# Kernel optimization log

Measured on AMD Instinct MI355X. Metric: run time of the kernel, lower is better.

The kernel has to match this reference:

```python
import jax, jax.numpy as jnp
import numpy as np

B, L, E, H, DV, V = 256, 512, 200, 256, 30000, 50000
NEG_INF = -jnp.inf

def setup_inputs() -> dict:
    key = jax.random.key(0)
    ks = jax.random.split(key, 16)
    s = 0.05
    f = jnp.float32
    return {
        "input_id": jax.random.randint(ks[0], (B, 1), 0, V),
        "input_emb": jax.random.normal(ks[1], (B, 1, E), f),
        "encoder_outputs": jax.random.normal(ks[2], (B, L, H), f),
        "encoder_input_ids": jax.random.randint(ks[3], (B, L), 0, V),
        "hidden": jax.random.normal(ks[4], (B, 1, H), f),
        "attention": jax.random.normal(ks[5], (B, 1, H), f),
        # GRU (PyTorch layout): W_ih (3H, 2H+E), W_hh (3H, H), gate order r,z,n
        "W_ih": jax.random.normal(ks[6], (3 * H, 2 * H + E), f) * s,
        "W_hh": jax.random.normal(ks[7], (3 * H, H), f) * s,
        "b_ih": jnp.zeros((3 * H,), f),
        "b_hh": jnp.zeros((3 * H,), f),
        "W_attn": jax.random.normal(ks[8], (H, H), f) * s,
        "b_attn": jnp.zeros((H,), f),
        "W_comb": jax.random.normal(ks[9], (H, 2 * H), f) * s,
        "b_comb": jnp.zeros((H,), f),
        "W_gen": jax.random.normal(ks[10], (DV, H), f) * s,
        "b_gen": jnp.zeros((DV,), f),
        "W_copy": jax.random.normal(ks[11], (H, H), f) * s,
        "b_copy": jnp.zeros((H,), f),
    }


def reference(input_id, input_emb, encoder_outputs, encoder_input_ids, hidden,
              attention, W_ih, W_hh, b_ih, b_hh, W_attn, b_attn, W_comb,
              b_comb, W_gen, b_gen, W_copy, b_copy):
    b, l = encoder_input_ids.shape
    # selective read: rou = normalized match mask (NaN guard -> 0)
    mask = (input_id == encoder_input_ids).astype(encoder_outputs.dtype)  # (b,l)
    msum = jnp.sum(mask, axis=1, keepdims=True)
    rou = jnp.where(msum > 0, mask / jnp.where(msum > 0, msum, 1.0), 0.0)
    selective_read = jnp.einsum('bl,blh->bh', rou, encoder_outputs)  # (b,h)

    # GRU single step (dropout is identity at inference)
    x = jnp.concatenate([input_emb[:, 0], attention[:, 0], selective_read], axis=-1)
    h_prev = hidden[:, 0]  # (b,h)
    gx = x @ W_ih.T + b_ih          # (b,3h)
    gh = h_prev @ W_hh.T + b_hh     # (b,3h)
    xr, xz, xn = jnp.split(gx, 3, axis=-1)
    hr, hz, hn = jnp.split(gh, 3, axis=-1)
    r = jax.nn.sigmoid(xr + hr)
    z = jax.nn.sigmoid(xz + hz)
    n = jnp.tanh(xn + r * hn)
    h = (1.0 - z) * n + z * h_prev  # (b,h) cur_hidden

    # attention
    q = h @ W_attn.T + b_attn
    attn_w = jax.nn.softmax(jnp.einsum('bh,blh->bl', q, encoder_outputs), axis=-1)
    attn_applied = jnp.einsum('bl,blh->bh', attn_w, encoder_outputs)
    cur_attention = jnp.tanh(
        jnp.concatenate([attn_applied, h], axis=-1) @ W_comb.T + b_comb)  # (b,h)

    # generate + copy scores, joint softmax
    generate_score = cur_attention @ W_gen.T + b_gen                     # (b,DV)
    copy_weights = jax.nn.sigmoid(encoder_outputs @ W_copy.T + b_copy)   # (b,l,h)
    copy_score = jnp.einsum('blh,bh->bl', copy_weights, cur_attention)   # (b,l)
    score = jax.nn.softmax(jnp.concatenate([generate_score, copy_score], axis=1), axis=1)
    gen_s, copy_s = score[:, :DV], score[:, DV:]

    # fused equivalent of the one-hot scatter/mix: direct scatter-add into vocab
    output = jnp.zeros((b, V), score.dtype)
    output = output.at[:, :DV].add(gen_s)
    output = output.at[jnp.arange(b)[:, None], encoder_input_ids].add(copy_s)

    pos = output > 0
    out = jnp.where(pos, jnp.log(jnp.where(pos, output, 1.0)), NEG_INF)
    return out, h[:, None, :], cur_attention[:, None, :]
```

## Files before the change

kernel.cpp:

```cpp
#include <hip/hip_runtime.h>
#include <cmath>

#define B_  256
#define L_  512
#define E_  200
#define H_  256
#define DV_ 30000
#define V_  50000
#define X_  712
#define G3_ 768
#define NT_ 235

#define NEG_BIG -1.0e30f

typedef __attribute__((ext_vector_type(8))) _Float16 half8;
typedef __attribute__((ext_vector_type(4))) float   floatx4;

#define GLOAD16(gptr, lptr)                                                            \
    __builtin_amdgcn_global_load_lds(                                                  \
        (const __attribute__((address_space(1))) unsigned int*)(gptr),                 \
        (__attribute__((address_space(3))) unsigned int*)(lptr), 16, 0, 0)

__global__ void k_selread(const int* __restrict__ input_id, const float* __restrict__ emb,
                          const float* __restrict__ attention, const float* __restrict__ hidden,
                          const float* __restrict__ enc, const int* __restrict__ enc_ids,
                          const float* __restrict__ Wc, _Float16* __restrict__ wcb,
                          float* __restrict__ xT) {
    int b = blockIdx.x, t = threadIdx.x;
    __shared__ int cnt;
    __shared__ int list[L_];
    if (t == 0) cnt = 0;
    __syncthreads();
    wcb[b * H_ + t] = (_Float16)Wc[b * H_ + t];
    int id = input_id[b];
    for (int l = t; l < L_; l += 256) {
        if (enc_ids[b * L_ + l] == id) { int p = atomicAdd(&cnt, 1); list[p] = l; }
    }
    __syncthreads();
    int n = cnt;
    float s = 0.f;
    for (int i = 0; i < n; i++) s += enc[(b * L_ + list[i]) * H_ + t];
    float sel = (n > 0) ? s / (float)n : 0.f;
    for (int k = t; k < E_; k += 256) xT[k * B_ + b] = emb[b * E_ + k];
    xT[(E_ + t) * B_ + b]       = attention[b * H_ + t];
    xT[(E_ + H_ + t) * B_ + b]  = sel;
    xT[(X_ + t) * B_ + b]       = hidden[b * H_ + t];
}

template<int K, int OS>
__global__ void __launch_bounds__(256) k_gru_one(const float* __restrict__ xTp, const float* __restrict__ W,
                                                 const float* __restrict__ bias, float* __restrict__ g) {
    __shared__ __align__(16) float Ws[8 * K];
    int t  = threadIdx.x;
    int j0 = blockIdx.x * 8;
    int bq = t & 63;
    int jh = t >> 6;
#pragma unroll
    for (int jj = 0; jj < 8; jj++) {
        const float4* src = (const float4*)(W + (size_t)(j0 + jj) * K);
        float4* dst = (float4*)(Ws + jj * K);
        for (int i = t; i < K / 4; i += 256) dst[i] = src[i];
    }
    __syncthreads();
    float acc0[4] = {0.f, 0.f, 0.f, 0.f};
    float acc1[4] = {0.f, 0.f, 0.f, 0.f};
    const float* w0 = Ws + (jh * 2 + 0) * K;
    const float* w1 = Ws + (jh * 2 + 1) * K;
#pragma unroll 2
    for (int k4 = 0; k4 < K / 4; k4++) {
        float4 wa = *(const float4*)(w0 + k4 * 4);
        float4 wb = *(const float4*)(w1 + k4 * 4);
        float wav[4] = {wa.x, wa.y, wa.z, wa.w};
        float wbv[4] = {wb.x, wb.y, wb.z, wb.w};
#pragma unroll
        for (int u = 0; u < 4; u++) {
            float4 xv = *(const float4*)(xTp + (size_t)(k4 * 4 + u) * B_ + bq * 4);
            acc0[0] += wav[u] * xv.x; acc0[1] += wav[u] * xv.y;
            acc0[2] += wav[u] * xv.z; acc0[3] += wav[u] * xv.w;
            acc1[0] += wbv[u] * xv.x; acc1[1] += wbv[u] * xv.y;
            acc1[2] += wbv[u] * xv.z; acc1[3] += wbv[u] * xv.w;
        }
    }
    int ja = j0 + jh * 2, jb = ja + 1;
    float ba = bias[ja], bb = bias[jb];
#pragma unroll
    for (int i = 0; i < 4; i++) {
        g[(size_t)(bq * 4 + i) * OS + ja] = acc0[i] + ba;
        g[(size_t)(bq * 4 + i) * OS + jb] = acc1[i] + bb;
    }
}

__global__ void k_gru_gates(const float* __restrict__ gx, const float* __restrict__ gh,
                            const float* __restrict__ hidden, float* __restrict__ hws,
                            float* __restrict__ hT, float* __restrict__ hout) {
    int b = blockIdx.x, j = threadIdx.x;
    float xr = gx[b * G3_ + j], xz = gx[b * G3_ + 256 + j], xn = gx[b * G3_ + 512 + j];
    float hr = gh[b * G3_ + j], hz = gh[b * G3_ + 256 + j], hn = gh[b * G3_ + 512 + j];
    float r = 1.f / (1.f + expf(-(xr + hr)));
    float z = 1.f / (1.f + expf(-(xz + hz)));
    float n = tanhf(xn + r * hn);
    float hp = hidden[b * H_ + j];
    float h = (1.f - z) * n + z * hp;
    hws[b * H_ + j] = h;
    hT[j * B_ + b]  = h;
    hout[b * H_ + j] = h;
}

#define NC_ 4
#define CR_ 128
__global__ void __launch_bounds__(256) k_attn_a(const float* __restrict__ qws, const float* __restrict__ enc,
                         float* __restrict__ avp, float* __restrict__ mdp) {
    int blk = blockIdx.x;
    int b = blk >> 2, c = blk & 3;
    int t = threadIdx.x, lane = t & 63, w = t >> 6;
    __shared__ float ps[CR_];
    __shared__ float red[8];
    const float* encc = enc + ((size_t)b * L_ + c * CR_) * H_;
    float4 q4 = *(const float4*)&qws[b * H_ + lane * 4];
    for (int i = 0; i < 32; i += 8) {
        float s[8];
#pragma unroll
        for (int u = 0; u < 8; u++) {
            float4 e = *(const float4*)(encc + (size_t)(w * 32 + i + u) * H_ + lane * 4);
            s[u] = q4.x * e.x + q4.y * e.y + q4.z * e.z + q4.w * e.w;
        }
#pragma unroll
        for (int u = 0; u < 8; u++) {
#pragma unroll
            for (int o = 1; o < 64; o <<= 1) s[u] += __shfl_xor(s[u], o);
            if (lane == 0) ps[w * 32 + i + u] = s[u];
        }
    }
    __syncthreads();
    {
        float v = ps[w * 32 + (lane & 31)];
#pragma unroll
        for (int o = 1; o < 64; o <<= 1) v = fmaxf(v, __shfl_xor(v, o));
        if (lane == 0) red[w] = v;
    }
    __syncthreads();
    float M = fmaxf(fmaxf(red[0], red[1]), fmaxf(red[2], red[3]));
    float e = (t < CR_) ? __expf(ps[t] - M) : 0.f;
    {
        float ssum = e;
#pragma unroll
        for (int o = 1; o < 64; o <<= 1) ssum += __shfl_xor(ssum, o);
        if (lane == 0) red[4 + w] = ssum;
    }
    __syncthreads();
    if (t < CR_) ps[t] = e;
    if (t == 0) {
        mdp[blk * 2]     = M;
        mdp[blk * 2 + 1] = red[4] + red[5] + red[6] + red[7];
    }
    __syncthreads();
    float a0 = 0.f, a1 = 0.f, a2 = 0.f, a3 = 0.f;
#pragma unroll 4
    for (int r = 0; r < CR_; r += 4) {
        a0 += ps[r + 0] * encc[(size_t)(r + 0) * H_ + t];
        a1 += ps[r + 1] * encc[(size_t)(r + 1) * H_ + t];
        a2 += ps[r + 2] * encc[(size_t)(r + 2) * H_ + t];
        a3 += ps[r + 3] * encc[(size_t)(r + 3) * H_ + t];
    }
    avp[(size_t)blk * H_ + t] = (a0 + a1) + (a2 + a3);
}

__global__ void __launch_bounds__(256) k_attn_b(const float* __restrict__ avp, const float* __restrict__ mdp,
                         const float* __restrict__ hws, const float* __restrict__ W_comb,
                         const float* __restrict__ b_comb,
                         float* __restrict__ caws, _Float16* __restrict__ cab,
                         float* __restrict__ caout) {
    int b = blockIdx.x, t = threadIdx.x;
    __shared__ __align__(16) float xs[2 * H_];
    float m0 = mdp[(b * 4 + 0) * 2], d0 = mdp[(b * 4 + 0) * 2 + 1];
    float m1 = mdp[(b * 4 + 1) * 2], d1 = mdp[(b * 4 + 1) * 2 + 1];
    float m2 = mdp[(b * 4 + 2) * 2], d2 = mdp[(b * 4 + 2) * 2 + 1];
    float m3 = mdp[(b * 4 + 3) * 2], d3 = mdp[(b * 4 + 3) * 2 + 1];
    float M = fmaxf(fmaxf(m0, m1), fmaxf(m2, m3));
    float f0 = __expf(m0 - M), f1 = __expf(m1 - M), f2 = __expf(m2 - M), f3 = __expf(m3 - M);
    float den = f0 * d0 + f1 * d1 + f2 * d2 + f3 * d3;
    float num = f0 * avp[((size_t)b * 4 + 0) * H_ + t] + f1 * avp[((size_t)b * 4 + 1) * H_ + t]
              + f2 * avp[((size_t)b * 4 + 2) * H_ + t] + f3 * avp[((size_t)b * 4 + 3) * H_ + t];
    xs[t]      = num / den;
    xs[H_ + t] = hws[b * H_ + t];
    __syncthreads();
    const float4* wr = (const float4*)(W_comb + (size_t)t * (2 * H_));
    const float4* xp = (const float4*)xs;
    float acc = 0.f;
#pragma unroll 8
    for (int k4 = 0; k4 < 128; k4++) {
        float4 wv = wr[k4], xv = xp[k4];
        acc += wv.x * xv.x + wv.y * xv.y + wv.z * xv.z + wv.w * xv.w;
    }
    float cav = tanhf(b_comb[t] + acc);
    caws[b * H_ + t]  = cav;
    cab[b * H_ + t]   = (_Float16)cav;
    caout[b * H_ + t] = cav;
}

__global__ void __launch_bounds__(256, 2) k_gen_mfma(
        const _Float16* __restrict__ cab, const float* __restrict__ W_gen,
        const float* __restrict__ b_gen, float* __restrict__ out,
        float2* __restrict__ pmd) {
    __shared__ __align__(16) _Float16 Ah[128 * 32];
    __shared__ __align__(16) float    Bf[128 * 32];
    __shared__ float mm[4][128], dd[4][128];
    int t = threadIdx.x, w = t >> 6, lane = t & 63;
    int n0 = blockIdx.x * 128, m0 = blockIdx.y * 128;
    int wm = (w >> 1) * 64, wn = (w & 1) * 64;
    int l15 = lane & 15, q = lane >> 4;
    floatx4 acc[4][4];
#pragma unroll
    for (int i = 0; i < 4; i++)
#pragma unroll
        for (int j = 0; j < 4; j++) acc[i][j] = (floatx4){0.f, 0.f, 0.f, 0.f};

    for (int kc = 0; kc < H_; kc += 32) {
#pragma unroll
        for (int i = 0; i < 2; i++) {
            int t2 = w * 2 + i;
            int row = t2 * 16 + (lane >> 2);
            const _Float16* g = cab + (size_t)(m0 + row) * H_ + kc + (lane & 3) * 8;
            GLOAD16(g, &Ah[t2 * 512]);
        }
#pragma unroll
        for (int i = 0; i < 4; i++) {
            int t2 = w * 4 + i;
            int row = t2 * 8 + (lane >> 3);
            int nn = n0 + row; nn = nn < DV_ ? nn : DV_ - 1;
            const float* g = W_gen + (size_t)nn * H_ + kc + (lane & 7) * 4;
            GLOAD16(g, &Bf[t2 * 256]);
        }
        __syncthreads();
        half8 a[4];
#pragma unroll
        for (int mi = 0; mi < 4; mi++) {
            int m = wm + mi * 16 + l15;
            a[mi] = *(const half8*)&Ah[m * 32 + q * 8];
        }
#pragma unroll
        for (int ni = 0; ni < 4; ni++) {
            int n = wn + ni * 16 + l15;
            const float4* bp = (const float4*)&Bf[n * 32 + q * 8];
            float4 f0 = bp[0], f1 = bp[1];
            half8 bf;
            bf[0] = (_Float16)f0.x; bf[1] = (_Float16)f0.y; bf[2] = (_Float16)f0.z; bf[3] = (_Float16)f0.w;
            bf[4] = (_Float16)f1.x; bf[5] = (_Float16)f1.y; bf[6] = (_Float16)f1.z; bf[7] = (_Float16)f1.w;
#pragma unroll
            for (int mi = 0; mi < 4; mi++)
                acc[mi][ni] = __builtin_amdgcn_mfma_f32_16x16x32_f16(a[mi], bf, acc[mi][ni], 0, 0, 0);
        }
        __syncthreads();
    }
    float bgs[4];
#pragma unroll
    for (int ni = 0; ni < 4; ni++) {
        int col = n0 + wn + ni * 16 + l15;
        if (col < DV_) {
            float bg = b_gen[col];
            bgs[ni] = bg;
#pragma unroll
            for (int mi = 0; mi < 4; mi++)
#pragma unroll
                for (int j = 0; j < 4; j++) {
                    int row = m0 + wm + mi * 16 + q * 4 + j;
                    out[(size_t)row * V_ + col] = acc[mi][ni][j] + bg;
                }
        } else bgs[ni] = 0.f;
    }
#pragma unroll
    for (int mi = 0; mi < 4; mi++)
#pragma unroll
        for (int j = 0; j < 4; j++) {
            float m_l = -INFINITY, d_l = 0.f;
#pragma unroll
            for (int ni = 0; ni < 4; ni++) {
                int col = n0 + wn + ni * 16 + l15;
                float v = (col < DV_) ? acc[mi][ni][j] + bgs[ni] : NEG_BIG;
                float mn = fmaxf(m_l, v);
                d_l = d_l * __expf(m_l - mn) + __expf(v - mn);
                m_l = mn;
            }
#pragma unroll
            for (int o = 1; o < 16; o <<= 1) {
                float m2 = __shfl_xor(m_l, o), d2 = __shfl_xor(d_l, o);
                float mn = fmaxf(m_l, m2);
                d_l = d_l * __expf(m_l - mn) + d2 * __expf(m2 - mn);
                m_l = mn;
            }
            if (l15 == 0) {
                int rl = wm + mi * 16 + q * 4 + j;
                mm[w][rl] = m_l; dd[w][rl] = d_l;
            }
        }
    __syncthreads();
    if (t < 128) {
        int wa = (t < 64) ? 0 : 2;
        float ma = mm[wa][t],     da = dd[wa][t];
        float mb = mm[wa + 1][t], db = dd[wa + 1][t];
        float M = fmaxf(ma, mb);
        float D = da * __expf(ma - M) + db * __expf(mb - M);
        pmd[(size_t)(m0 + t) * NT_ + blockIdx.x] = make_float2(M, D);
    }
}

__global__ void __launch_bounds__(256, 2) k_copy_mfma(
        const float* __restrict__ enc, const _Float16* __restrict__ wcb,
        const float* __restrict__ b_copy, const float* __restrict__ caws,
        float* __restrict__ copy_s) {
    __shared__ __align__(16) float    Af[128 * 32];
    __shared__ __align__(16) _Float16 Bh[256 * 32];
    __shared__ float bcs[H_], cas[H_];
    int t = threadIdx.x, w = t >> 6, lane = t & 63;
    int R0 = blockIdx.x * 128;
    int b  = blockIdx.x >> 2;
    int l15 = lane & 15, q = lane >> 4;
    bcs[t] = b_copy[t];
    cas[t] = caws[b * H_ + t];
    floatx4 acc[2][16];
#pragma unroll
    for (int i = 0; i < 2; i++)
#pragma unroll
        for (int j = 0; j < 16; j++) acc[i][j] = (floatx4){0.f, 0.f, 0.f, 0.f};

    for (int kc = 0; kc < H_; kc += 32) {
#pragma unroll
        for (int i = 0; i < 4; i++) {
            int t2 = w * 4 + i;
            int row = t2 * 8 + (lane >> 3);
            const float* g = enc + (size_t)(R0 + row) * H_ + kc + (lane & 7) * 4;
            GLOAD16(g, &Af[t2 * 256]);
        }
#pragma unroll
        for (int i = 0; i < 4; i++) {
            int t2 = w * 4 + i;
            int row = t2 * 16 + (lane >> 2);
            const _Float16* g = wcb + row * H_ + kc + (lane & 3) * 8;
            GLOAD16(g, &Bh[t2 * 512]);
        }
        __syncthreads();
        half8 a[2];
#pragma unroll
        for (int mi = 0; mi < 2; mi++) {
            int m = w * 32 + mi * 16 + l15;
            const float4* apx = (const float4*)&Af[m * 32 + q * 8];
            float4 f0 = apx[0], f1 = apx[1];
            half8 h;
            h[0] = (_Float16)f0.x; h[1] = (_Float16)f0.y; h[2] = (_Float16)f0.z; h[3] = (_Float16)f0.w;
            h[4] = (_Float16)f1.x; h[5] = (_Float16)f1.y; h[6] = (_Float16)f1.z; h[7] = (_Float16)f1.w;
            a[mi] = h;
        }
#pragma unroll
        for (int ni = 0; ni < 16; ni++) {
            int n = ni * 16 + l15;
            half8 bf = *(const half8*)&Bh[n * 32 + q * 8];
            acc[0][ni] = __builtin_amdgcn_mfma_f32_16x16x32_f16(a[0], bf, acc[0][ni], 0, 0, 0);
            acc[1][ni] = __builtin_amdgcn_mfma_f32_16x16x32_f16(a[1], bf, acc[1][ni], 0, 0, 0);
        }
        __syncthreads();
    }
#pragma unroll
    for (int mi = 0; mi < 2; mi++) {
#pragma unroll
        for (int j = 0; j < 4; j++) {
            float p = 0.f;
#pragma unroll
            for (int ni = 0; ni < 16; ni++) {
                int col = ni * 16 + l15;
                float v = acc[mi][ni][j] + bcs[col];
                p += cas[col] / (1.f + __expf(-v));
            }
            p += __shfl_xor(p, 1);
            p += __shfl_xor(p, 2);
            p += __shfl_xor(p, 4);
            p += __shfl_xor(p, 8);
            if (l15 == 0) copy_s[R0 + w * 32 + mi * 16 + q * 4 + j] = p;
        }
    }
}

__global__ void __launch_bounds__(256) k_stats2(const float2* __restrict__ pmd, const float* __restrict__ copy_s,
                         float* __restrict__ mrow, float* __restrict__ ldrow) {
    int b = blockIdx.x, t = threadIdx.x, lane = t & 63, w = t >> 6;
    __shared__ float rm[4], rs[4];
    float m = -INFINITY, d = 0.f;
    if (t < NT_) { float2 p = pmd[(size_t)b * NT_ + t]; m = p.x; d = p.y; }
    float v0 = copy_s[b * L_ + t];
    float v1 = copy_s[b * L_ + 256 + t];
    float mn = fmaxf(m, v0); d = d * __expf(m - mn) + __expf(v0 - mn); m = mn;
    mn = fmaxf(m, v1); d = d * __expf(m - mn) + __expf(v1 - mn); m = mn;
#pragma unroll
    for (int o = 1; o < 64; o <<= 1) {
        float m2 = __shfl_xor(m, o), d2 = __shfl_xor(d, o);
        mn = fmaxf(m, m2);
        d = d * __expf(m - mn) + d2 * __expf(m2 - mn);
        m = mn;
    }
    if (lane == 0) { rm[w] = m; rs[w] = d; }
    __syncthreads();
    if (t == 0) {
        float M = rm[0], S = rs[0];
        for (int i = 1; i < 4; i++) {
            float mx = fmaxf(M, rm[i]);
            S = S * __expf(M - mx) + rs[i] * __expf(rm[i] - mx);
            M = mx;
        }
        mrow[b] = M;
        ldrow[b] = __logf(S);
    }
}

__global__ void __launch_bounds__(256) k_final(float* __restrict__ out, const float* __restrict__ mrow,
                        const float* __restrict__ ldrow) {
    int idx = blockIdx.x * 256 + threadIdx.x;
    int b = blockIdx.y;
    if (idx >= V_ / 4) return;
    float4* o4 = (float4*)(out + (size_t)b * V_) + idx;
    if (idx >= DV_ / 4) {
        *o4 = make_float4(NEG_BIG, NEG_BIG, NEG_BIG, NEG_BIG);
        return;
    }
    float sh = mrow[b] + ldrow[b];
    float4 v = *o4;
    v.x -= sh; v.y -= sh; v.z -= sh; v.w -= sh;
    *o4 = v;
}

__global__ void k_scatter_log(float* __restrict__ out, const float* __restrict__ copy_s,
                              const int* __restrict__ enc_ids, const float* __restrict__ mrow,
                              const float* __restrict__ ldrow) {
    int l = blockIdx.x * 256 + threadIdx.x;
    int b = blockIdx.y;
    float p = __expf(copy_s[b * L_ + l] - mrow[b] - ldrow[b]);
    unsigned int* up = (unsigned int*)(out + (size_t)b * V_ + enc_ids[b * L_ + l]);
    unsigned int cur = *up;
    while (true) {
        float ov = __uint_as_float(cur);
        float pv = (ov < -1.0e29f) ? p : __expf(ov) + p;
        unsigned int prev = atomicCAS(up, cur, __float_as_uint(__logf(pv)));
        if (prev == cur) break;
        cur = prev;
    }
}

extern "C" void kernel_launch(void* const* d_in, const int* in_sizes, int n_in,
                              void* d_out, int out_size, void* d_ws, size_t ws_size,
                              hipStream_t stream) {
    const int*   input_id  = (const int*)  d_in[0];
    const float* input_emb = (const float*)d_in[1];
    const float* enc       = (const float*)d_in[2];
    const int*   enc_ids   = (const int*)  d_in[3];
    const float* hidden    = (const float*)d_in[4];
    const float* attention = (const float*)d_in[5];
    const float* W_ih      = (const float*)d_in[6];
    const float* W_hh      = (const float*)d_in[7];
    const float* b_ih      = (const float*)d_in[8];
    const float* b_hh      = (const float*)d_in[9];
    const float* W_attn    = (const float*)d_in[10];
    const float* b_attn    = (const float*)d_in[11];
    const float* W_comb    = (const float*)d_in[12];
    const float* b_comb    = (const float*)d_in[13];
    const float* W_gen     = (const float*)d_in[14];
    const float* b_gen     = (const float*)d_in[15];
    const float* W_copy    = (const float*)d_in[16];
    const float* b_copy    = (const float*)d_in[17];

    float* out = (float*)d_out;
    float* ws  = (float*)d_ws;
    float* xT   = ws;
    float* gx   = xT + 247808;
    float* gh   = gx + 196608;
    float* hws  = gh + 196608;
    float* caws = hws + 65536;
    float* cps  = caws + 65536;
    float* mrow = cps + 131072;
    float* ldrow = mrow + 256;
    _Float16* wcb = (_Float16*)(ldrow + 256);
    _Float16* cab = wcb + 65536;
    float* qws  = (float*)(cab + 65536);
    float* mdp  = qws + 65536;
    float2* pmd = (float2*)(mdp + 2048);
    float* hT   = xT;
    float* avp  = gx;

    float* hout  = out + (size_t)B_ * V_;
    float* caout = hout + B_ * H_;

    k_selread<<<256, 256, 0, stream>>>(input_id, input_emb, attention, hidden, enc, enc_ids, W_copy, wcb, xT);
    k_gru_one<712, G3_><<<96, 256, 0, stream>>>(xT, W_ih, b_ih, gx);
    k_gru_one<256, G3_><<<96, 256, 0, stream>>>(xT + X_ * B_, W_hh, b_hh, gh);
    k_gru_gates<<<256, 256, 0, stream>>>(gx, gh, hidden, hws, hT, hout);
    k_gru_one<256, H_><<<32, 256, 0, stream>>>(hT, W_attn, b_attn, qws);
    k_attn_a<<<B_ * NC_, 256, 0, stream>>>(qws, enc, avp, mdp);
    k_attn_b<<<256, 256, 0, stream>>>(avp, mdp, hws, W_comb, b_comb, caws, cab, caout);
    k_gen_mfma<<<dim3(NT_, 2), 256, 0, stream>>>(cab, W_gen, b_gen, out, pmd);
    k_copy_mfma<<<(B_ * L_) / 128, 256, 0, stream>>>(enc, wcb, b_copy, caws, cps);
    k_stats2<<<256, 256, 0, stream>>>(pmd, cps, mrow, ldrow);
    dim3 gf((V_ / 4 + 255) / 256, B_);
    k_final<<<gf, 256, 0, stream>>>(out, mrow, ldrow);
    dim3 gs(L_ / 256, B_);
    k_scatter_log<<<gs, 256, 0, stream>>>(out, cps, enc_ids, mrow, ldrow);
}
```

Baseline: 481.2 us.

## Swizzle LDS tiles in MFMA GEMMs and vectorize attention weighted sum

XOR-swizzles the 16-byte chunk positions when global_load_lds writes the A and B tiles of the generate and copy MFMA kernels, and applies the matching swizzle on the LDS reads. This is meant to remove LDS bank conflicts on the row-strided 16-byte reads. Separately, the attention-applied sum in k_attn_a now has each wave handle 32 rows with float4 loads, then reduces the four partial results through shared memory. That adds one barrier and 4KB of LDS in exchange for wider, more coalesced encoder reads.

```diff
diff --git a/kernel.cpp b/kernel.cpp
--- a/kernel.cpp
+++ b/kernel.cpp
@@ -115,6 +115,7 @@
     int t = threadIdx.x, lane = t & 63, w = t >> 6;
     __shared__ float ps[CR_];
     __shared__ float red[8];
+    __shared__ __align__(16) float pavs[4][H_];
     const float* encc = enc + ((size_t)b * L_ + c * CR_) * H_;
     float4 q4 = *(const float4*)&qws[b * H_ + lane * 4];
     for (int i = 0; i < 32; i += 8) {
@@ -154,15 +155,20 @@
         mdp[blk * 2 + 1] = red[4] + red[5] + red[6] + red[7];
     }
     __syncthreads();
-    float a0 = 0.f, a1 = 0.f, a2 = 0.f, a3 = 0.f;
+    {
+        float4 av = {0.f, 0.f, 0.f, 0.f};
+        const float* encg = encc + (size_t)w * 32 * H_;
+        const float* psg  = &ps[w * 32];
 #pragma unroll 4
-    for (int r = 0; r < CR_; r += 4) {
-        a0 += ps[r + 0] * encc[(size_t)(r + 0) * H_ + t];
-        a1 += ps[r + 1] * encc[(size_t)(r + 1) * H_ + t];
-        a2 += ps[r + 2] * encc[(size_t)(r + 2) * H_ + t];
-        a3 += ps[r + 3] * encc[(size_t)(r + 3) * H_ + t];
-    }
-    avp[(size_t)blk * H_ + t] = (a0 + a1) + (a2 + a3);
+        for (int r = 0; r < 32; r++) {
+            float p = psg[r];
+            float4 ev = *(const float4*)(encg + (size_t)r * H_ + lane * 4);
+            av.x += p * ev.x; av.y += p * ev.y; av.z += p * ev.z; av.w += p * ev.w;
+        }
+        *(float4*)&pavs[w][lane * 4] = av;
+    }
+    __syncthreads();
+    avp[(size_t)blk * H_ + t] = pavs[0][t] + pavs[1][t] + pavs[2][t] + pavs[3][t];
 }
 
 __global__ void __launch_bounds__(256) k_attn_b(const float* __restrict__ avp, const float* __restrict__ mdp,
@@ -220,15 +226,17 @@
         for (int i = 0; i < 2; i++) {
             int t2 = w * 2 + i;
             int row = t2 * 16 + (lane >> 2);
-            const _Float16* g = cab + (size_t)(m0 + row) * H_ + kc + (lane & 3) * 8;
+            int sl  = (lane & 3) ^ ((row >> 1) & 3);
+            const _Float16* g = cab + (size_t)(m0 + row) * H_ + kc + sl * 8;
             GLOAD16(g, &Ah[t2 * 512]);
         }
 #pragma unroll
         for (int i = 0; i < 4; i++) {
             int t2 = w * 4 + i;
             int row = t2 * 8 + (lane >> 3);
+            int sl  = (lane & 7) ^ (row & 7);
             int nn = n0 + row; nn = nn < DV_ ? nn : DV_ - 1;
-            const float* g = W_gen + (size_t)nn * H_ + kc + (lane & 7) * 4;
+            const float* g = W_gen + (size_t)nn * H_ + kc + sl * 4;
             GLOAD16(g, &Bf[t2 * 256]);
         }
         __syncthreads();
@@ -236,13 +244,14 @@
 #pragma unroll
         for (int mi = 0; mi < 4; mi++) {
             int m = wm + mi * 16 + l15;
-            a[mi] = *(const half8*)&Ah[m * 32 + q * 8];
+            a[mi] = *(const half8*)&Ah[m * 32 + (q ^ ((m >> 1) & 3)) * 8];
         }
 #pragma unroll
         for (int ni = 0; ni < 4; ni++) {
             int n = wn + ni * 16 + l15;
-            const float4* bp = (const float4*)&Bf[n * 32 + q * 8];
-            float4 f0 = bp[0], f1 = bp[1];
+            const float* bb = &Bf[n * 32];
+            float4 f0 = *(const float4*)&bb[((q * 2 + 0) ^ (n & 7)) * 4];
+            float4 f1 = *(const float4*)&bb[((q * 2 + 1) ^ (n & 7)) * 4];
             half8 bf;
             bf[0] = (_Float16)f0.x; bf[1] = (_Float16)f0.y; bf[2] = (_Float16)f0.z; bf[3] = (_Float16)f0.w;
             bf[4] = (_Float16)f1.x; bf[5] = (_Float16)f1.y; bf[6] = (_Float16)f1.z; bf[7] = (_Float16)f1.w;
@@ -328,14 +337,16 @@
         for (int i = 0; i < 4; i++) {
             int t2 = w * 4 + i;
             int row = t2 * 8 + (lane >> 3);
-            const float* g = enc + (size_t)(R0 + row) * H_ + kc + (lane & 7) * 4;
+            int sl  = (lane & 7) ^ (row & 7);
+            const float* g = enc + (size_t)(R0 + row) * H_ + kc + sl * 4;
             GLOAD16(g, &Af[t2 * 256]);
         }
 #pragma unroll
         for (int i = 0; i < 4; i++) {
             int t2 = w * 4 + i;
             int row = t2 * 16 + (lane >> 2);
-            const _Float16* g = wcb + row * H_ + kc + (lane & 3) * 8;
+            int sl  = (lane & 3) ^ ((row >> 1) & 3);
+            const _Float16* g = wcb + row * H_ + kc + sl * 8;
             GLOAD16(g, &Bh[t2 * 512]);
         }
         __syncthreads();
@@ -343,8 +354,9 @@
 #pragma unroll
         for (int mi = 0; mi < 2; mi++) {
             int m = w * 32 + mi * 16 + l15;
-            const float4* apx = (const float4*)&Af[m * 32 + q * 8];
-            float4 f0 = apx[0], f1 = apx[1];
+            const float* ar = &Af[m * 32];
+            float4 f0 = *(const float4*)&ar[((q * 2 + 0) ^ (m & 7)) * 4];
+            float4 f1 = *(const float4*)&ar[((q * 2 + 1) ^ (m & 7)) * 4];
             half8 h;
             h[0] = (_Float16)f0.x; h[1] = (_Float16)f0.y; h[2] = (_Float16)f0.z; h[3] = (_Float16)f0.w;
             h[4] = (_Float16)f1.x; h[5] = (_Float16)f1.y; h[6] = (_Float16)f1.z; h[7] = (_Float16)f1.w;
@@ -353,7 +365,7 @@
 #pragma unroll
         for (int ni = 0; ni < 16; ni++) {
             int n = ni * 16 + l15;
-            half8 bf = *(const half8*)&Bh[n * 32 + q * 8];
+            half8 bf = *(const half8*)&Bh[n * 32 + (q ^ ((n >> 1) & 3)) * 8];
             acc[0][ni] = __builtin_amdgcn_mfma_f32_16x16x32_f16(a[0], bf, acc[0][ni], 0, 0, 0);
             acc[1][ni] = __builtin_amdgcn_mfma_f32_16x16x32_f16(a[1], bf, acc[1][ni], 0, 0, 0);
         }
```

Result: faster. 447.6 us (-7.0%).
